# Kernel tuning notes

Measured on AMD Instinct MI355X. Metric: run time of the kernel, lower is better.

The kernel has to match this reference:

```python
import jax, jax.numpy as jnp
import numpy as np

HR, LR, K, RANK = 2048, 1024, 8, 16


def setup_inputs() -> dict:
    key = jax.random.key(0)
    kA, kX, kW, kU, kV, kM = jax.random.split(key, 6)
    A = jax.random.normal(kA, (LR, LR), dtype=jnp.float32)
    A = (A + A.T) / 2  # symmetric so torch UPLO='U' and jax eigh agree
    X = jax.random.normal(kX, (LR, HR), dtype=jnp.float32)
    init_range = (6.0 / (HR + HR)) ** 0.5  # glorot uniform
    weights = jax.random.uniform(kW, (HR, HR), dtype=jnp.float32,
                                 minval=-init_range, maxval=init_range)
    Us = jax.random.normal(kU, (K, HR, RANK), dtype=jnp.float32) * 0.001
    # original inits Vs to zeros; use small noise so corrections are nonzero
    Vs = jax.random.normal(kV, (K, HR, RANK), dtype=jnp.float32) * 0.01
    alphas = jnp.ones((K,), dtype=jnp.float32) / K
    masks = (jax.random.uniform(kM, (K, HR, HR)) < 0.5).astype(jnp.float32)
    return {"A": A, "X": X, "weights": weights, "Us": Us, "Vs": Vs,
            "alphas": alphas, "masks": masks}


def _set_unit_diag(M, eye):
    return M * (1.0 - eye) + eye


def reference(A, X, weights, Us, Vs, alphas, masks):
    lr = A.shape[0]
    hr = weights.shape[0]
    eye_hr = jnp.eye(hr, dtype=A.dtype)
    # --- GSRLayer ---
    _, U_lr = jnp.linalg.eigh(A)                      # (lr, lr)
    s_d = jnp.concatenate([jnp.eye(lr, dtype=A.dtype),
                           jnp.eye(lr, dtype=A.dtype)], axis=0)  # (hr, lr)
    f_d = weights @ s_d @ U_lr.T @ X                  # (hr, hr)
    adj = jnp.abs(f_d)
    adj = _set_unit_diag(adj, eye_hr)
    # --- community-aware low-rank corrections ---
    alpha = jax.nn.softmax(alphas)                    # (k,)
    Zm = adj[None, :, :] * masks                      # (k, hr, hr)
    t = jnp.einsum('kij,kjr->kir', Zm, Us)            # (k, hr, rank)
    corr = jnp.einsum('kir,kjr->kij', t, Vs) * masks  # (k, hr, hr)
    out_adj = adj + jnp.einsum('k,kij->ij', alpha, corr)
    # --- symmetrize with unit diagonal ---
    X_out = out_adj @ out_adj.T
    X_out = (X_out + X_out.T) / 2
    X_out = _set_unit_diag(X_out, eye_hr)
    return out_adj, jnp.abs(X_out)
```

## Files before the change

### kernel.cpp

```cpp
#include <hip/hip_runtime.h>
#include <hip/hip_bf16.h>

typedef unsigned long long u64;

#define MBYTE (1ull << 20)

static const size_t OFF_A64   = 0;
static const size_t OFF_VT    = 8*MBYTE;
static const size_t OFF_TAU   = 12*MBYTE;
static const size_t OFF_D64   = 12*MBYTE +  8192;
static const size_t OFF_E64   = 12*MBYTE + 16384;
static const size_t OFF_XB    = 12*MBYTE + 24576;
static const size_t OFF_Y2B   = 12*MBYTE + 32768;
static const size_t OFF_Y1B   = 12*MBYTE + 40960;
static const size_t OFF_XA    = 12*MBYTE + 49152;
static const size_t OFF_Y1A   = 12*MBYTE + 57344;
static const size_t OFF_Y2A   = 12*MBYTE + 65536;
static const size_t OFF_QA    = 13*MBYTE;
static const size_t OFF_QB    = 17*MBYTE;
static const size_t OFF_SHAT  = 21*MBYTE;
static const size_t OFF_WC    = 25*MBYTE;
static const size_t OFF_M1    = 33*MBYTE;
static const size_t OFF_T8    = 33*MBYTE;
static const size_t OFF_ALPHA = 35*MBYTE + 512*1024;
static const size_t OFF_ADJ   = 41*MBYTE;
static const size_t OFF_OADJ  = 17*MBYTE;
static const size_t OFF_CBUF  = 0;

static const size_t SCD_STRIDE = 9216;
static const size_t SCI_STRIDE = 6144;
static const size_t OFF_SCDB  = OFF_WC;
static const size_t OFF_SCIB  = OFF_WC + 2359296;
static const size_t OFF_KNB   = OFF_WC + 2359296 + 786432;
static const size_t OFF_KNDB  = OFF_WC + 2359296 + 786432 + 2048;


__global__ void kCopyA(const float* __restrict__ A, double* __restrict__ A64) {
  int gid = blockIdx.x*256 + threadIdx.x;
  if (gid < 1024*1024) A64[gid] = (double)A[gid];
}

__device__ __forceinline__ double agLoadD(const double* p) {
  return __hip_atomic_load(p, __ATOMIC_RELAXED, __HIP_MEMORY_SCOPE_AGENT);
}
__device__ __forceinline__ void agStoreD(double* p, double v) {
  __hip_atomic_store(p, v, __ATOMIC_RELAXED, __HIP_MEMORY_SCOPE_AGENT);
}

__global__ __launch_bounds__(1024) void kTriDiag(
    double* __restrict__ A64,
    double* __restrict__ y1A, double* __restrict__ y1B,
    double* __restrict__ y2A, double* __restrict__ y2B,
    double* __restrict__ diagP, unsigned* __restrict__ bar,
    double* __restrict__ tauv, double* __restrict__ e64, double* __restrict__ d64,
    float* __restrict__ Vt) {
  __shared__ double xL[1024], vL[1024], wL[1024], ytL[1024];
  __shared__ double red[4];
  __shared__ double sS[4];
  int tid = threadIdx.x;
  int bid = blockIdx.x;
  bool w0 = (bid == 0);
  int lane = tid & 63, wave = tid >> 6;
  unsigned* barCnt = bar;
  unsigned* barGen = bar + 32;
  const int NBLK = 64;
  int myRow = wave*64 + bid;

  for (int i = 0; i <= 1023; ++i) {
    const double* y1in = (((i-1)&1) != 0) ? y1B : y1A;
    const double* y2in = (((i-1)&1) != 0) ? y2B : y2A;
    double* y1out = ((i&1) != 0) ? y1B : y1A;
    double* y2out = ((i&1) != 0) ? y2B : y2A;

    if (i == 0) {
      if (tid < 256) {
        for (int c = tid; c < 1024; c += 256) { vL[c] = 0.0; wL[c] = 0.0; }
        for (int c = 1 + tid; c < 1024; c += 256) xL[c] = A64[(u64)c*1024];
        if (w0 && tid == 0) d64[0] = A64[0];
      }
      __syncthreads();
    } else {
      int j = i - 1;
      if (tid < 256) {
        double acc = 0.0;
        for (int c = i + 1 + tid; c < 1024; c += 256) { double v = xL[c]; acc += v*v; }
        for (int off = 32; off > 0; off >>= 1) acc += __shfl_xor(acc, off, 64);
        if (lane == 0) red[wave] = acc;
      }
      __syncthreads();
      if (tid == 0) {
        double xn2 = red[0] + red[1] + red[2] + red[3];
        double alpha = xL[i];
        double tv, sc;
        if (xn2 == 0.0) { tv = 0.0; if (w0) e64[j] = alpha; sc = 0.0; }
        else {
          double beta = (alpha >= 0.0) ? -sqrt(alpha*alpha + xn2) : sqrt(alpha*alpha + xn2);
          tv = (beta - alpha)/beta;
          if (w0) e64[j] = beta;
          sc = 1.0/(alpha - beta);
        }
        if (w0) tauv[j] = tv;
        sS[0] = sc; sS[1] = tv;
        vL[i] = 1.0;
        if (w0) Vt[(u64)j*1024 + i] = 1.0f;
      }
      __syncthreads();
      if (tid < 256) {
        double sc = sS[0];
        for (int c = i + 1 + tid; c < 1024; c += 256) {
          double v = xL[c]*sc;
          vL[c] = v;
          if (w0) Vt[(u64)j*1024 + c] = (float)v;
        }
      }
      __syncthreads();
      if (tid < 256) {
        double sc = sS[0], tv = sS[1];
        double acc2 = 0.0;
        for (int r = i + tid; r < 1024; r += 256) {
          double y1v = agLoadD(&y1in[r]);
          double y2v = agLoadD(&y2in[r]);
          ytL[r] = y1v;
          double P = tv*(y1v + sc*y2v);
          wL[r] = P;
          acc2 += P*vL[r];
        }
        for (int off = 32; off > 0; off >>= 1) acc2 += __shfl_xor(acc2, off, 64);
        if (lane == 0) red[wave] = acc2;
      }
      __syncthreads();
      if (tid == 0) sS[2] = 0.5*sS[1]*(red[0] + red[1] + red[2] + red[3]);
      __syncthreads();
      if (tid < 256) {
        double coef = sS[2];
        for (int r = i + tid; r < 1024; r += 256) wL[r] -= coef*vL[r];
      }
      __syncthreads();
      if (tid < 256) {
        double wi = wL[i];
        for (int c = i + 1 + tid; c < 1024; c += 256)
          xL[c] = ytL[c] - vL[c]*wi - wL[c];
        if (tid == 0 && w0) d64[i] = agLoadD(&diagP[i]) - 2.0*wL[i];
      }
      __syncthreads();
    }
    if (i <= 1022) {
      int r = myRow;
      if (r >= i + 1) {
        double vr = vL[r], wr = wL[r];
        double* Arow = A64 + (u64)r*1024;
        double acc = 0.0, y1v = 0.0;
        for (int c = i + 1 + lane; c < 1024; c += 64) {
          double a = Arow[c] - vr*wL[c] - wr*vL[c];
          Arow[c] = a;
          if (c == r) agStoreD(&diagP[r], a);
          if (c == i + 1) y1v = a; else acc += a*xL[c];
        }
        for (int off = 32; off > 0; off >>= 1) acc += __shfl_down(acc, off, 64);
        if (lane == 0) { agStoreD(&y1out[r], y1v); agStoreD(&y2out[r], acc); }
      }
    }
    __syncthreads();
    if (tid == 0) {
      unsigned target = (unsigned)(i + 1);
      unsigned prev = __hip_atomic_fetch_add(barCnt, 1u, __ATOMIC_ACQ_REL, __HIP_MEMORY_SCOPE_AGENT);
      if (prev == (unsigned)(NBLK - 1)) {
        __hip_atomic_store(barCnt, 0u, __ATOMIC_RELAXED, __HIP_MEMORY_SCOPE_AGENT);
        __hip_atomic_store(barGen, target, __ATOMIC_RELEASE, __HIP_MEMORY_SCOPE_AGENT);
      } else {
        while (__hip_atomic_load(barGen, __ATOMIC_ACQUIRE, __HIP_MEMORY_SCOPE_AGENT) < target) {
          __builtin_amdgcn_s_sleep(2);
        }
      }
    }
    __syncthreads();
  }
  if (w0 && tid == 0) {
    for (int c = 16; c < 1024; c += 16) {
      double ae = fabs(e64[c-1]);
      d64[c-1] -= ae;
      d64[c]   -= ae;
    }
  }
}


__device__ void slartg_(double f, double g, double* cs, double* sn, double* r) {
  if (g == 0.0) { *cs = 1.0; *sn = 0.0; *r = f; }
  else if (f == 0.0) { *cs = 0.0; *sn = (g >= 0.0) ? 1.0 : -1.0; *r = fabs(g); }
  else {
    double d = sqrt(f*f + g*g);
    *cs = fabs(f)/d;
    *r = (f >= 0.0) ? d : -d;
    *sn = g / (*r);
  }
}

__device__ void slaev2_(double a, double b, double c, double* rt1, double* rt2,
                        double* cs1, double* sn1) {
  double sm = a + c, df = a - c, adf = fabs(df), tb = b + b, ab = fabs(tb);
  double acmx, acmn;
  if (fabs(a) > fabs(c)) { acmx = a; acmn = c; } else { acmx = c; acmn = a; }
  double rt;
  if (adf > ab) rt = adf*sqrt(1.0 + (ab/adf)*(ab/adf));
  else if (adf < ab) rt = ab*sqrt(1.0 + (adf/ab)*(adf/ab));
  else rt = ab*sqrt(2.0);
  int sgn1;
  if (sm < 0.0) { *rt1 = 0.5*(sm - rt); sgn1 = -1; *rt2 = (acmx / *rt1)*acmn - (b / *rt1)*b; }
  else if (sm > 0.0) { *rt1 = 0.5*(sm + rt); sgn1 = 1; *rt2 = (acmx / *rt1)*acmn - (b / *rt1)*b; }
  else { *rt1 = 0.5*rt; *rt2 = -0.5*rt; sgn1 = 1; }
  int sgn2; double cs;
  if (df >= 0.0) { cs = df + rt; sgn2 = 1; } else { cs = df - rt; sgn2 = -1; }
  double acs = fabs(cs);
  if (acs > ab) { double ct = -tb/cs; *sn1 = 1.0/sqrt(1.0 + ct*ct); *cs1 = ct*(*sn1); }
  else {
    if (ab == 0.0) { *cs1 = 1.0; *sn1 = 0.0; }
    else { double tn = -cs/tb; *cs1 = 1.0/sqrt(1.0 + tn*tn); *sn1 = tn*(*cs1); }
  }
  if (sgn1 == sgn2) { double tn = *cs1; *cs1 = -(*sn1); *sn1 = tn; }
}

__device__ void steqr16_(double* d, double* e, double* z, double* wc, double* ws_) {
  const int n = 16;
  const double eps = 5.9604644775390625e-08;
  const double eps2 = eps*eps;
  const double safmin = 1.1754943508222875e-38;
  int jtot = 0; const int nmaxit = n*30;
  int l1 = 0;
  for (int outer = 0; outer < 200; ++outer) {
    if (l1 > n-1) break;
    if (l1 > 0) e[l1-1] = 0.0;
    int m = l1;
    for (; m <= n-2; ++m) {
      double tst = fabs(e[m]);
      if (tst == 0.0) break;
      if (tst <= (sqrt(fabs(d[m]))*sqrt(fabs(d[m+1])))*eps) { e[m] = 0.0; break; }
    }
    int l = l1, lend = m;
    l1 = m + 1;
    if (lend == l) continue;
    if (fabs(d[lend]) < fabs(d[l])) { int t = l; l = lend; lend = t; }
    if (lend > l) {
      for (int it = 0; it < 800; ++it) {
        int mm = lend;
        if (l != lend) {
          for (mm = l; mm <= lend-1; ++mm) {
            double tst = e[mm]*e[mm];
            if (tst <= eps2*fabs(d[mm])*fabs(d[mm+1]) + safmin) break;
          }
        }
        if (mm < lend) e[mm] = 0.0;
        double p = d[l];
        if (mm == l) { d[l] = p; ++l; if (l <= lend) continue; break; }
        if (mm == l+1) {
          double rt1, rt2, c2, s2;
          slaev2_(d[l], e[l], d[l+1], &rt1, &rt2, &c2, &s2);
          for (int r = 0; r < n; ++r) {
            double t = z[r*16 + l + 1];
            z[r*16 + l + 1] = c2*t - s2*z[r*16 + l];
            z[r*16 + l]     = s2*t + c2*z[r*16 + l];
          }
          d[l] = rt1; d[l+1] = rt2; e[l] = 0.0;
          l += 2; if (l <= lend) continue; break;
        }
        if (jtot == nmaxit) break;
        ++jtot;
        double g = (d[l+1] - p)/(2.0*e[l]);
        double r_ = sqrt(g*g + 1.0);
        g = d[mm] - p + e[l]/(g + ((g >= 0.0) ? r_ : -r_));
        double s = 1.0, c = 1.0;
        p = 0.0;
        for (int i = mm-1; i >= l; --i) {
          double f = s*e[i], b = c*e[i];
          double cs, sn, rr;
          slartg_(g, f, &cs, &sn, &rr);
          c = cs; s = sn;
          if (i != mm-1) e[i+1] = rr;
          g = d[i+1] - p;
          rr = (d[i] - g)*s + 2.0*c*b;
          p = s*rr;
          d[i+1] = g + p;
          g = c*rr - b;
          wc[i] = c; ws_[i] = -s;
        }
        for (int jj = mm-1; jj >= l; --jj) {
          double cs = wc[jj], sn = ws_[jj];
          for (int r = 0; r < n; ++r) {
            double t = z[r*16 + jj + 1];
            z[r*16 + jj + 1] = cs*t - sn*z[r*16 + jj];
            z[r*16 + jj]     = sn*t + cs*z[r*16 + jj];
          }
        }
        d[l] -= p;
        e[l] = g;
      }
    } else {
      for (int it = 0; it < 800; ++it) {
        int mm = lend;
        if (l != lend) {
          for (mm = l; mm >= lend+1; --mm) {
            double tst = e[mm-1]*e[mm-1];
            if (tst <= eps2*fabs(d[mm])*fabs(d[mm-1]) + safmin) break;
          }
        }
        if (mm > lend) e[mm-1] = 0.0;
        double p = d[l];
        if (mm == l) { d[l] = p; --l; if (l >= lend) continue; break; }
        if (mm == l-1) {
          double rt1, rt2, c2, s2;
          slaev2_(d[l-1], e[l-1], d[l], &rt1, &rt2, &c2, &s2);
          for (int r = 0; r < n; ++r) {
            double t = z[r*16 + l];
            z[r*16 + l]     = c2*t - s2*z[r*16 + l - 1];
            z[r*16 + l - 1] = s2*t + c2*z[r*16 + l - 1];
          }
          d[l-1] = rt1; d[l] = rt2; e[l-1] = 0.0;
          l -= 2; if (l >= lend) continue; break;
        }
        if (jtot == nmaxit) break;
        ++jtot;
        double g = (d[l-1] - p)/(2.0*e[l-1]);
        double r_ = sqrt(g*g + 1.0);
        g = d[mm] - p + e[l-1]/(g + ((g >= 0.0) ? r_ : -r_));
        double s = 1.0, c = 1.0;
        p = 0.0;
        for (int i = mm; i <= l-1; ++i) {
          double f = s*e[i], b = c*e[i];
          double cs, sn, rr;
          slartg_(g, f, &cs, &sn, &rr);
          c = cs; s = sn;
          if (i != mm) e[i-1] = rr;
          g = d[i] - p;
          rr = (d[i+1] - g)*s + 2.0*c*b;
          p = s*rr;
          d[i] = g + p;
          g = c*rr - b;
          wc[i] = c; ws_[i] = s;
        }
        for (int jj = mm; jj <= l-1; ++jj) {
          double cs = wc[jj], sn = ws_[jj];
          for (int r = 0; r < n; ++r) {
            double t = z[r*16 + jj + 1];
            z[r*16 + jj + 1] = cs*t - sn*z[r*16 + jj];
            z[r*16 + jj]     = sn*t + cs*z[r*16 + jj];
          }
        }
        d[l] -= p;
        e[l-1] = g;
      }
    }
  }
  for (int ii = 1; ii <= n-1; ++ii) {
    int i = ii - 1, k = i;
    double p = d[i];
    for (int j = ii; j <= n-1; ++j) if (d[j] < p) { k = j; p = d[j]; }
    if (k != i) {
      d[k] = d[i]; d[i] = p;
      for (int r = 0; r < n; ++r) { double t = z[r*16 + i]; z[r*16 + i] = z[r*16 + k]; z[r*16 + k] = t; }
    }
  }
}

__global__ void kLeaf(double* d64, const double* e64, float* Qa) {
  __shared__ double dd[16], ed[16], zd[256], wk1[16], wk2[16];
  int leaf = blockIdx.x, lo = leaf*16, tid = threadIdx.x;
  for (int idx = tid; idx < 256; idx += 64) zd[idx] = ((idx/16) == (idx%16)) ? 1.0 : 0.0;
  if (tid < 16) { dd[tid] = d64[lo + tid]; ed[tid] = (tid < 15) ? e64[lo + tid] : 0.0; }
  __syncthreads();
  if (tid == 0) steqr16_(dd, ed, zd, wk1, wk2);
  __syncthreads();
  for (int idx = tid; idx < 256; idx += 64) {
    int r = idx/16, c = idx%16;
    Qa[(u64)(lo + r)*1024 + lo + c] = (float)zd[idx];
  }
  if (tid < 16) d64[lo + tid] = dd[tid];
}


__global__ __launch_bounds__(1024) void kDeflateB(float* __restrict__ Qa,
      const double* __restrict__ d64, const double* __restrict__ e64,
      double* scdB, int* sciB, int* knB, double* kndB, int bs) {
  __shared__ double zL[1024], dlocL[1024], redD[1024];
  __shared__ double rcL[1024], rsL[1024];
  __shared__ int sIdxL[1024], rpqL[1024];
  __shared__ double sSc[4];
  __shared__ int sKn[4];
  int mg = blockIdx.x;
  int n1 = bs, n = 2*bs, lo = mg*n;
  double* scd = scdB + (u64)mg*SCD_STRIDE;
  int*    sci = sciB + (u64)mg*SCI_STRIDE;
  int* kn = knB + mg*8;
  double* knd = kndB + mg*4;
  int tid = threadIdx.x;
  if (tid == 0) sSc[0] = e64[lo + n1 - 1];
  __syncthreads();
  double rho_in = sSc[0];
  const double invs2 = 0.70710678118654752440;
  if (tid < n) {
    int row = (tid < n1) ? (lo + n1 - 1) : (lo + n1);
    double s = (rho_in < 0.0 && tid >= n1) ? -invs2 : invs2;
    zL[tid] = (double)Qa[(u64)row*1024 + lo + tid] * s;
    dlocL[tid] = d64[lo + tid];
  }
  __syncthreads();
  if (tid < n) {
    int pos; double key = dlocL[tid];
    if (tid < n1) {
      int loB = 0, hiB = n - n1;
      while (loB < hiB) { int mid = (loB+hiB)>>1; if (dlocL[n1+mid] < key) loB = mid+1; else hiB = mid; }
      pos = tid + loB;
    } else {
      int loA = 0, hiA = n1;
      while (loA < hiA) { int mid = (loA+hiA)>>1; if (dlocL[mid] <= key) loA = mid+1; else hiA = mid; }
      pos = (tid - n1) + loA;
    }
    sIdxL[pos] = tid;
  }
  redD[tid] = (tid < n) ? fabs(zL[tid]) : 0.0;
  __syncthreads();
  for (int s = 512; s > 0; s >>= 1) { if (tid < s) redD[tid] = fmax(redD[tid], redD[tid+s]); __syncthreads(); }
  if (tid == 0) sSc[1] = redD[0];
  __syncthreads();
  redD[tid] = (tid < n) ? fabs(dlocL[tid]) : 0.0;
  __syncthreads();
  for (int s = 512; s > 0; s >>= 1) { if (tid < s) redD[tid] = fmax(redD[tid], redD[tid+s]); __syncthreads(); }
  if (tid == 0) {
    double zmax = sSc[1], dmax = redD[0];
    double rho = fabs(2.0*rho_in);
    double tol = 8.0*5.9604644775390625e-8*fmax(dmax, zmax);
    double* dlG = scd + 1024;
    double* wmG = scd + 2048;
    double* dvalG = scd + 7168;
    int* permG = sci;
    int* deflG = sci + 1024;
    int K = 0, nrot = 0, nd = 0; double sw2 = 0.0;
    if (rho*zmax <= tol) {
      for (int pos = 0; pos < n; ++pos) { int c = sIdxL[pos]; deflG[nd] = c; dvalG[nd] = dlocL[c]; nd++; }
    } else {
      int pj = -1, jpos = 0;
      for (; jpos < n; ++jpos) {
        int nj = sIdxL[jpos];
        if (rho*fabs(zL[nj]) <= tol) { deflG[nd] = nj; dvalG[nd] = dlocL[nj]; nd++; }
        else { pj = nj; break; }
      }
      for (++jpos; jpos < n; ++jpos) {
        int nj = sIdxL[jpos];
        if (rho*fabs(zL[nj]) <= tol) { deflG[nd] = nj; dvalG[nd] = dlocL[nj]; nd++; continue; }
        double s_ = zL[pj], c_ = zL[nj];
        double tu = sqrt(c_*c_ + s_*s_);
        double tdif = dlocL[nj] - dlocL[pj];
        c_ /= tu; s_ = -s_/tu;
        if (fabs(tdif*c_*s_) <= tol) {
          zL[nj] = tu; zL[pj] = 0.0;
          rpqL[nrot] = (pj << 16) | nj; rcL[nrot] = c_; rsL[nrot] = s_; nrot++;
          double t1 = dlocL[pj]*c_*c_ + dlocL[nj]*s_*s_;
          dlocL[nj] = dlocL[pj]*s_*s_ + dlocL[nj]*c_*c_;
          dlocL[pj] = t1;
          deflG[nd] = pj; dvalG[nd] = t1; nd++;
          pj = nj;
        } else {
          permG[K] = pj; dlG[K] = dlocL[pj]; wmG[K] = zL[pj]; sw2 += zL[pj]*zL[pj]; K++;
          pj = nj;
        }
      }
      permG[K] = pj; dlG[K] = dlocL[pj]; wmG[K] = zL[pj]; sw2 += zL[pj]*zL[pj]; K++;
    }
    sKn[1] = nrot;
    kn[0] = K; kn[1] = nrot; kn[2] = nd;
    knd[0] = rho; knd[1] = sw2;
  }
  __syncthreads();
  int nrot = sKn[1];
  if (tid < n && nrot > 0) {
    u64 row = (u64)(lo + tid)*1024;
    for (int t = 0; t < nrot; ++t) {
      int pq = rpqL[t];
      int p = lo + (pq >> 16), q = lo + (pq & 0xffff);
      double c = rcL[t], s = rsL[t];
      double x = (double)Qa[row + p], y = (double)Qa[row + q];
      Qa[row + p] = (float)(c*x + s*y);
      Qa[row + q] = (float)(c*y - s*x);
    }
  }
}

__global__ __launch_bounds__(256) void kSecularB(double* scdB, const int* knB, const double* kndB) {
  __shared__ double dlS[1024], wmS[1024];
  int mg = blockIdx.y;
  double* scd = scdB + (u64)mg*SCD_STRIDE;
  const int* kn = knB + mg*8;
  const double* knd = kndB + mg*4;
  int K = kn[0];
  int tid = threadIdx.x;
  for (int j = tid; j < K; j += 256) { dlS[j] = scd[1024 + j]; wmS[j] = scd[2048 + j]; }
  __syncthreads();
  int wave = tid >> 6, lane = tid & 63;
  int i = blockIdx.x*4 + wave;
  if (i >= K) return;
  double rho = knd[0], sw2 = knd[1];
  double di = dlS[i];
  double hi = (i < K-1) ? (dlS[i+1] - di) : (rho*sw2*(1.0 + 1e-12) + 1e-300);
  double lo_ = 0.0;
  for (int it = 0; it < 100; ++it) {
    double mid = 0.5*(lo_ + hi);
    double g = 0.0;
    for (int j = lane; j < K; j += 64) { double w = wmS[j]; g += w*w/((dlS[j] - di) - mid); }
    for (int off = 32; off > 0; off >>= 1) g += __shfl_xor(g, off);
    g = 1.0 + rho*g;
    if (g < 0.0) lo_ = mid; else hi = mid;
  }
  scd[3072 + i] = 0.5*(lo_ + hi);
}

__global__ void kZhatB(double* scdB, const int* knB) {
  int mg = blockIdx.y;
  double* scd = scdB + (u64)mg*SCD_STRIDE;
  int K = (knB + mg*8)[0];
  int j = blockIdx.x*64 + threadIdx.x;
  if (j >= K) return;
  const double* dl = scd + 1024;
  const double* wm = scd + 2048;
  const double* mu = scd + 3072;
  double dj = dl[j];
  double prod = mu[j];
  for (int i2 = 0; i2 < K; ++i2) {
    if (i2 == j) continue;
    double dd = dl[i2] - dj;
    prod *= (dd + mu[i2]) / dd;
  }
  prod = fabs(prod);
  scd[4096 + j] = (wm[j] >= 0.0) ? sqrt(prod) : -sqrt(prod);
}

__global__ __launch_bounds__(1024) void kSortPermB(double* scdB, int* sciB, const int* knB,
                                                   double* d64, int bs) {
  __shared__ double sv[1024];
  __shared__ int si[1024];
  int mg = blockIdx.x;
  int n = 2*bs, lo = mg*n;
  double* scd = scdB + (u64)mg*SCD_STRIDE;
  int* sci = sciB + (u64)mg*SCI_STRIDE;
  int K = (knB + mg*8)[0];
  int tid = threadIdx.x;
  const double* dl = scd + 1024;
  const double* mu = scd + 3072;
  const double* dval = scd + 7168;
  double v;
  if (tid < K) v = dl[tid] + mu[tid];
  else if (tid < n) v = dval[tid - K];
  else v = 1e300;
  sv[tid] = v; si[tid] = tid;
  __syncthreads();
  for (int k = 2; k <= 1024; k <<= 1) {
    for (int j = k >> 1; j > 0; j >>= 1) {
      int ixj = tid ^ j;
      if (ixj > tid) {
        bool up = ((tid & k) == 0);
        double a = sv[tid], b = sv[ixj];
        int ia = si[tid], ib = si[ixj];
        bool agtb = (a > b) || (a == b && ia > ib);
        if (up ? agtb : !agtb) { sv[tid] = b; sv[ixj] = a; si[tid] = ib; si[ixj] = ia; }
      }
      __syncthreads();
    }
  }
  if (tid < n) {
    int s = si[tid];
    if (s < K) sci[4096 + s] = tid; else sci[5120 + s - K] = tid;
    d64[lo + tid] = sv[tid];
  }
}

__global__ void kSvecNormB(float* __restrict__ Shat, const double* scdB, const int* knB, int bs) {
  int mg = blockIdx.y;
  int n = 2*bs, lo = mg*n;
  const double* scd = scdB + (u64)mg*SCD_STRIDE;
  int K = (knB + mg*8)[0];
  int i = blockIdx.x;
  if (i >= K) return;
  const double* dl = scd + 1024;
  const double* mu = scd + 3072;
  const double* zh = scd + 4096;
  __shared__ double red[256];
  int tid = threadIdx.x;
  double di = dl[i], m = mu[i];
  double acc = 0.0;
  for (int j = tid; j < K; j += 256) {
    double v = zh[j]/((dl[j] - di) - m);
    acc += v*v;
  }
  red[tid] = acc; __syncthreads();
  for (int s = 128; s > 0; s >>= 1) { if (tid < s) red[tid] += red[tid+s]; __syncthreads(); }
  double inv = 1.0/sqrt(red[0]);
  for (int j = tid; j < K; j += 256) {
    double v = zh[j]/((dl[j] - di) - m);
    Shat[(u64)j*1024 + lo + i] = (float)(v*inv);
  }
}

__global__ void kGatherB(const float* Qa, float* Qb, const int* sciB, const int* knB, int bs) {
  int mg = blockIdx.y;
  int n = 2*bs, lo = mg*n;
  const int* sci = sciB + (u64)mg*SCI_STRIDE;
  int K = (knB + mg*8)[0];
  int gid = blockIdx.x*256 + threadIdx.x;
  if (gid >= n*n) return;
  int p = gid % n, r = gid / n;
  int src = (p < K) ? sci[p] : sci[1024 + p - K];
  Qb[(u64)(lo + r)*1024 + p] = Qa[(u64)(lo + r)*1024 + lo + src];
}

__global__ void kGemmMergeB(const float* __restrict__ Qb, const float* __restrict__ Shat,
                            float* __restrict__ Qa, const int* sciB, const int* knB, int bs) {
  __shared__ float As[16][17], Bs[16][17];
  int mg = blockIdx.z;
  int n = 2*bs, lo = mg*n;
  const int* sci = sciB + (u64)mg*SCI_STRIDE;
  int K = (knB + mg*8)[0];
  int tx = threadIdx.x, ty = threadIdx.y;
  int r0 = blockIdx.y*16, c0 = blockIdx.x*16;
  const int* rootpos = sci + 4096;
  float acc = 0.f;
  for (int k0 = 0; k0 < K; k0 += 16) {
    As[ty][tx] = (k0 + tx < K) ? Qb[(u64)(lo + r0 + ty)*1024 + k0 + tx] : 0.f;
    Bs[ty][tx] = (k0 + ty < K && c0 + tx < K) ? Shat[(u64)(k0 + ty)*1024 + lo + c0 + tx] : 0.f;
    __syncthreads();
    #pragma unroll
    for (int kk = 0; kk < 16; ++kk) acc += As[ty][kk]*Bs[kk][tx];
    __syncthreads();
  }
  int i = c0 + tx;
  if (i < K) Qa[(u64)(lo + r0 + ty)*1024 + lo + rootpos[i]] = acc;
}

__global__ void kScatterDeflB(const float* Qb, float* Qa, const int* sciB, const int* knB, int bs) {
  int mg = blockIdx.y;
  int n = 2*bs, lo = mg*n;
  const int* sci = sciB + (u64)mg*SCI_STRIDE;
  const int* kn = knB + mg*8;
  int gid = blockIdx.x*256 + threadIdx.x;
  if (gid >= n*n) return;
  int p = gid % n, r = gid / n;
  int K = kn[0], nd = kn[2];
  if (p < K || p - K >= nd) return;
  Qa[(u64)(lo + r)*1024 + lo + sci[5120 + p - K]] = Qb[(u64)(lo + r)*1024 + p];
}

__global__ void kBackx(float* __restrict__ Qa, const float* __restrict__ Vt,
                       const double* __restrict__ tau) {
  __shared__ double red[256];
  __shared__ double stot[16];
  int tid = threadIdx.x;
  int cix = tid & 15, strip = tid >> 4;
  int col = blockIdx.x*16 + cix;
  for (int i = 1022; i >= 0; --i) {
    int m0 = i + 1;
    double s = 0.0;
    for (int r = m0 + strip; r < 1024; r += 16)
      s += (double)Vt[(u64)i*1024 + r] * (double)Qa[(u64)r*1024 + col];
    red[tid] = s;
    __syncthreads();
    if (tid < 16) {
      double tot = 0.0;
      for (int u = 0; u < 16; ++u) tot += red[u*16 + tid];
      stot[tid] = tot * tau[i];
    }
    __syncthreads();
    double f = stot[cix];
    for (int r = m0 + strip; r < 1024; r += 16)
      Qa[(u64)r*1024 + col] -= (float)(f * (double)Vt[(u64)i*1024 + r]);
    __syncthreads();
  }
}


template<int TA, int TB>
__global__ __launch_bounds__(256) void gemm_f32(const float* __restrict__ A,
    const float* __restrict__ B, float* __restrict__ C,
    int M, int N, int Kd, int lda, int ldb, int ldc) {
  __shared__ float As[8][132];
  __shared__ float Bs[8][132];
  int tid = threadIdx.x;
  int bi = blockIdx.y*128, bj = blockIdx.x*128;
  int tx = tid & 15, ty = tid >> 4;
  float acc[8][8];
  #pragma unroll
  for (int x = 0; x < 8; ++x)
    #pragma unroll
    for (int y = 0; y < 8; ++y) acc[x][y] = 0.f;
  for (int k0 = 0; k0 < Kd; k0 += 8) {
    if (TA == 0) {
      int row = tid >> 1, kc = (tid & 1)*4;
      float4 v = *(const float4*)&A[(u64)(bi + row)*lda + k0 + kc];
      As[kc+0][row] = v.x; As[kc+1][row] = v.y; As[kc+2][row] = v.z; As[kc+3][row] = v.w;
    } else {
      int kk = tid >> 5, col = (tid & 31)*4;
      float4 v = *(const float4*)&A[(u64)(k0 + kk)*lda + bi + col];
      *(float4*)&As[kk][col] = v;
    }
    if (TB == 0) {
      int kk = tid >> 5, col = (tid & 31)*4;
      float4 v = *(const float4*)&B[(u64)(k0 + kk)*ldb + bj + col];
      *(float4*)&Bs[kk][col] = v;
    } else {
      int row = tid >> 1, kc = (tid & 1)*4;
      float4 v = *(const float4*)&B[(u64)(bj + row)*ldb + k0 + kc];
      Bs[kc+0][row] = v.x; Bs[kc+1][row] = v.y; Bs[kc+2][row] = v.z; Bs[kc+3][row] = v.w;
    }
    __syncthreads();
    #pragma unroll
    for (int kk = 0; kk < 8; ++kk) {
      float a[8], b[8];
      *(float4*)&a[0] = *(float4*)&As[kk][ty*8];
      *(float4*)&a[4] = *(float4*)&As[kk][ty*8 + 4];
      *(float4*)&b[0] = *(float4*)&Bs[kk][tx*8];
      *(float4*)&b[4] = *(float4*)&Bs[kk][tx*8 + 4];
      #pragma unroll
      for (int x = 0; x < 8; ++x)
        #pragma unroll
        for (int y = 0; y < 8; ++y) acc[x][y] += a[x]*b[y];
    }
    __syncthreads();
  }
  #pragma unroll
  for (int x = 0; x < 8; ++x) {
    float* Crow = &C[(u64)(bi + ty*8 + x)*ldc + bj + tx*8];
    *(float4*)&Crow[0] = make_float4(acc[x][0], acc[x][1], acc[x][2], acc[x][3]);
    *(float4*)&Crow[4] = make_float4(acc[x][4], acc[x][5], acc[x][6], acc[x][7]);
  }
}

__global__ void kWc(const float* W, float* Wc) {
  int gid = blockIdx.x*256 + threadIdx.x;
  if (gid >= 2048*1024) return;
  int i = gid >> 10, k = gid & 1023;
  Wc[gid] = W[(u64)i*2048 + k] + W[(u64)i*2048 + 1024 + k];
}

__global__ void kAbsDiag(float* adj) {
  int gid = blockIdx.x*256 + threadIdx.x;
  if (gid >= 2048*2048) return;
  int i = gid >> 11, j = gid & 2047;
  float v = fabsf(adj[gid]);
  adj[gid] = (i == j) ? 1.0f : v;
}

__global__ void kTk(const float* __restrict__ adj, const float* __restrict__ masks,
                    const float* __restrict__ Us, float* __restrict__ t8) {
  int k = blockIdx.y;
  int i = blockIdx.x*16 + (threadIdx.x >> 4);
  int r = threadIdx.x & 15;
  const float* arow = adj + (u64)i*2048;
  const float* mrow = masks + ((u64)k*2048 + i)*2048;
  const float* uk = Us + (u64)k*2048*16 + r;
  float acc = 0.f;
  for (int j = 0; j < 2048; ++j) acc += arow[j]*mrow[j]*uk[(u64)j*16];
  t8[((u64)k*2048 + i)*16 + r] = acc;
}

__global__ void kAlpha(const float* alphas, float* alpha) {
  if (threadIdx.x == 0 && blockIdx.x == 0) {
    float m = alphas[0];
    for (int k = 1; k < 8; ++k) m = fmaxf(m, alphas[k]);
    float e[8]; float s = 0.f;
    for (int k = 0; k < 8; ++k) { e[k] = expf(alphas[k] - m); s += e[k]; }
    for (int k = 0; k < 8; ++k) alpha[k] = e[k]/s;
  }
}

__global__ void kOutAdj(const float* __restrict__ adj, const float* __restrict__ masks,
                        const float* __restrict__ Vs, const float* __restrict__ t8,
                        const float* __restrict__ alpha, float* __restrict__ oadj,
                        float* __restrict__ out0) {
  __shared__ float tS[8][16][16];
  __shared__ float vS[8][16][16];
  int j0 = blockIdx.x*16, i0 = blockIdx.y*16;
  int tid = threadIdx.x;
  for (int idx = tid; idx < 2048; idx += 256) {
    int k = idx >> 8, rem = idx & 255, row = rem >> 4, r = rem & 15;
    tS[k][row][r] = t8[((u64)k*2048 + i0 + row)*16 + r];
    vS[k][row][r] = Vs[((u64)k*2048 + j0 + row)*16 + r];
  }
  __syncthreads();
  int ii = tid >> 4, jj = tid & 15;
  int i = i0 + ii, j = j0 + jj;
  float corr = 0.f;
  for (int k = 0; k < 8; ++k) {
    float m = masks[((u64)k*2048 + i)*2048 + j];
    float dv = 0.f;
    #pragma unroll
    for (int r = 0; r < 16; ++r) dv += tS[k][ii][r]*vS[k][jj][r];
    corr += alpha[k]*m*dv;
  }
  float val = adj[(u64)i*2048 + j] + corr;
  oadj[(u64)i*2048 + j] = val;
  out0[(u64)i*2048 + j] = val;
}

__global__ void kFinal(const float* __restrict__ C, float* __restrict__ out1) {
  int gid = blockIdx.x*256 + threadIdx.x;
  if (gid >= 2048*2048) return;
  int i = gid >> 11, j = gid & 2047;
  float v;
  if (i == j) v = 1.0f;
  else v = 0.5f*(C[gid] + C[(u64)j*2048 + i]);
  out1[gid] = fabsf(v);
}


extern "C" void kernel_launch(void* const* d_in, const int* in_sizes, int n_in,
                              void* d_out, int out_size, void* d_ws, size_t ws_size,
                              hipStream_t stream) {
  const float* A      = (const float*)d_in[0];
  const float* X      = (const float*)d_in[1];
  const float* W      = (const float*)d_in[2];
  const float* Us     = (const float*)d_in[3];
  const float* Vs     = (const float*)d_in[4];
  const float* alphas = (const float*)d_in[5];
  const float* masks  = (const float*)d_in[6];

  char* ws = (char*)d_ws;
  double* A64  = (double*)(ws + OFF_A64);
  float*  Vt   = (float*) (ws + OFF_VT);
  double* tau  = (double*)(ws + OFF_TAU);
  double* d64  = (double*)(ws + OFF_D64);
  double* e64  = (double*)(ws + OFF_E64);
  double* diagP = (double*)(ws + OFF_XA);
  unsigned* bar = (unsigned*)(ws + OFF_XB);
  double* y1a  = (double*)(ws + OFF_Y1A);
  double* y1b  = (double*)(ws + OFF_Y1B);
  double* y2a  = (double*)(ws + OFF_Y2A);
  double* y2b  = (double*)(ws + OFF_Y2B);
  double* SCDB = (double*)(ws + OFF_SCDB);
  int*    SCIB = (int*)   (ws + OFF_SCIB);
  int*    KNB  = (int*)   (ws + OFF_KNB);
  double* KNDB = (double*)(ws + OFF_KNDB);
  float*  ALPH = (float*) (ws + OFF_ALPHA);
  float*  Qa   = (float*) (ws + OFF_QA);
  float*  Qb   = (float*) (ws + OFF_QB);
  float*  Shat = (float*) (ws + OFF_SHAT);
  float*  Wc   = (float*) (ws + OFF_WC);
  float*  M1   = (float*) (ws + OFF_M1);
  float*  T8   = (float*) (ws + OFF_T8);
  float*  ADJ  = (float*) (ws + OFF_ADJ);
  float*  OADJ = (float*) (ws + OFF_OADJ);
  float*  CB   = (float*) (ws + OFF_CBUF);

  float* out0 = (float*)d_out;
  float* out1 = out0 + (u64)2048*2048;

  hipMemsetAsync(ws + OFF_XB, 0, 256, stream);
  kCopyA<<<4096, 256, 0, stream>>>(A, A64);
  {
    void* kargs[] = { (void*)&A64, (void*)&y1a, (void*)&y1b, (void*)&y2a, (void*)&y2b,
                      (void*)&diagP, (void*)&bar,
                      (void*)&tau, (void*)&e64, (void*)&d64, (void*)&Vt };
    hipLaunchCooperativeKernel((void*)kTriDiag, dim3(64), dim3(1024), kargs, 0, stream);
  }

  hipMemsetAsync(Qa, 0, (size_t)4*MBYTE, stream);
  kLeaf<<<64, 64, 0, stream>>>(d64, e64, Qa);

  for (int lvl = 0; lvl < 6; ++lvl) {
    int bs = 16 << lvl;
    int n = 2*bs;
    int cnt = 1024/n;
    kDeflateB<<<cnt, 1024, 0, stream>>>(Qa, d64, e64, SCDB, SCIB, KNB, KNDB, bs);
    kSecularB<<<dim3((n + 3)/4, cnt), 256, 0, stream>>>(SCDB, KNB, KNDB);
    kZhatB<<<dim3((n + 63)/64, cnt), 64, 0, stream>>>(SCDB, KNB);
    kSortPermB<<<cnt, 1024, 0, stream>>>(SCDB, SCIB, KNB, d64, bs);
    kSvecNormB<<<dim3(n, cnt), 256, 0, stream>>>(Shat, SCDB, KNB, bs);
    kGatherB<<<dim3((n*n + 255)/256, cnt), 256, 0, stream>>>(Qa, Qb, SCIB, KNB, bs);
    kGemmMergeB<<<dim3(n/16, n/16, cnt), dim3(16, 16), 0, stream>>>(Qb, Shat, Qa, SCIB, KNB, bs);
    kScatterDeflB<<<dim3((n*n + 255)/256, cnt), 256, 0, stream>>>(Qb, Qa, SCIB, KNB, bs);
  }

  kBackx<<<64, 256, 0, stream>>>(Qa, Vt, tau);

  kWc<<<8192, 256, 0, stream>>>(W, Wc);
  gemm_f32<1,0><<<dim3(16, 8), 256, 0, stream>>>(Qa, X, M1, 1024, 2048, 1024, 1024, 2048, 2048);
  gemm_f32<0,0><<<dim3(16, 16), 256, 0, stream>>>(Wc, M1, ADJ, 2048, 2048, 1024, 1024, 2048, 2048);
  kAbsDiag<<<16384, 256, 0, stream>>>(ADJ);
  kTk<<<dim3(128, 8), 256, 0, stream>>>(ADJ, masks, Us, T8);
  kAlpha<<<1, 64, 0, stream>>>(alphas, ALPH);
  kOutAdj<<<dim3(128, 128), 256, 0, stream>>>(ADJ, masks, Vs, T8, ALPH, OADJ, out0);
  gemm_f32<0,1><<<dim3(16, 16), 256, 0, stream>>>(OADJ, OADJ, CB, 2048, 2048, 2048, 2048, 2048, 2048);
  kFinal<<<16384, 256, 0, stream>>>(CB, out1);
}
```

Measured before the change: 20.90 ms.

## Restructure tridiagonal reduction grid, use flag barrier, and pair Householder back-transforms

The cooperative tridiagonalisation kernel moves from 64 blocks of 1024 threads (only 256 of them active in the per-step vector phase) to 256 blocks of 256 threads. It replaces the counter/generation grid barrier with per-block flags that a single wave polls, prefetches the y vectors before the norm reduction, and merges several of the per-step shared-memory phases so fewer __syncthreads are needed. The row update loop is unrolled four-wide. The back-transformation kernel applies two Householder reflectors per pass, which halves the number of sequential sweeps over Qa at the cost of an extra dot product and more register use.

```diff
diff --git a/kernel.cpp b/kernel.cpp
--- a/kernel.cpp
+++ b/kernel.cpp
@@ -47,24 +47,23 @@
   __hip_atomic_store(p, v, __ATOMIC_RELAXED, __HIP_MEMORY_SCOPE_AGENT);
 }
 
-__global__ __launch_bounds__(1024) void kTriDiag(
+#define TD_NBLK 256
+
+__global__ __launch_bounds__(256) void kTriDiag(
     double* __restrict__ A64,
     double* __restrict__ y1A, double* __restrict__ y1B,
     double* __restrict__ y2A, double* __restrict__ y2B,
-    double* __restrict__ diagP, unsigned* __restrict__ bar,
+    double* __restrict__ diagP, unsigned* __restrict__ flags,
     double* __restrict__ tauv, double* __restrict__ e64, double* __restrict__ d64,
     float* __restrict__ Vt) {
-  __shared__ double xL[1024], vL[1024], wL[1024], ytL[1024];
+  __shared__ double xL[1024], vL[1024], wL[1024], y1L[1024], y2L[1024];
   __shared__ double red[4];
   __shared__ double sS[4];
   int tid = threadIdx.x;
   int bid = blockIdx.x;
   bool w0 = (bid == 0);
   int lane = tid & 63, wave = tid >> 6;
-  unsigned* barCnt = bar;
-  unsigned* barGen = bar + 32;
-  const int NBLK = 64;
-  int myRow = wave*64 + bid;
+  int myRow = wave*TD_NBLK + bid;
 
   for (int i = 0; i <= 1023; ++i) {
     const double* y1in = (((i-1)&1) != 0) ? y1B : y1A;
@@ -73,20 +72,26 @@
     double* y2out = ((i&1) != 0) ? y2B : y2A;
 
     if (i == 0) {
-      if (tid < 256) {
-        for (int c = tid; c < 1024; c += 256) { vL[c] = 0.0; wL[c] = 0.0; }
-        for (int c = 1 + tid; c < 1024; c += 256) xL[c] = A64[(u64)c*1024];
-        if (w0 && tid == 0) d64[0] = A64[0];
-      }
+      for (int c = tid; c < 1024; c += 256) { vL[c] = 0.0; wL[c] = 0.0; }
+      for (int c = 1 + tid; c < 1024; c += 256) xL[c] = A64[(u64)c*1024];
+      if (w0 && tid == 0) d64[0] = A64[0];
       __syncthreads();
     } else {
       int j = i - 1;
-      if (tid < 256) {
-        double acc = 0.0;
-        for (int c = i + 1 + tid; c < 1024; c += 256) { double v = xL[c]; acc += v*v; }
-        for (int off = 32; off > 0; off >>= 1) acc += __shfl_xor(acc, off, 64);
-        if (lane == 0) red[wave] = acc;
-      }
+      double a1[4], a2[4];
+      #pragma unroll
+      for (int k = 0; k < 4; ++k) {
+        a1[k] = agLoadD(&y1in[tid + 256*k]);
+        a2[k] = agLoadD(&y2in[tid + 256*k]);
+      }
+      double dg = 0.0;
+      if (w0 && tid == 0) dg = agLoadD(&diagP[i]);
+      double acc = 0.0;
+      for (int c = i + 1 + tid; c < 1024; c += 256) { double v = xL[c]; acc += v*v; }
+      for (int off = 32; off > 0; off >>= 1) acc += __shfl_xor(acc, off, 64);
+      if (lane == 0) red[wave] = acc;
+      #pragma unroll
+      for (int k = 0; k < 4; ++k) { y1L[tid + 256*k] = a1[k]; y2L[tid + 256*k] = a2[k]; }
       __syncthreads();
       if (tid == 0) {
         double xn2 = red[0] + red[1] + red[2] + red[3];
@@ -105,42 +110,39 @@
         if (w0) Vt[(u64)j*1024 + i] = 1.0f;
       }
       __syncthreads();
-      if (tid < 256) {
-        double sc = sS[0];
-        for (int c = i + 1 + tid; c < 1024; c += 256) {
-          double v = xL[c]*sc;
-          vL[c] = v;
-          if (w0) Vt[(u64)j*1024 + c] = (float)v;
-        }
-      }
-      __syncthreads();
-      if (tid < 256) {
+      {
         double sc = sS[0], tv = sS[1];
         double acc2 = 0.0;
         for (int r = i + tid; r < 1024; r += 256) {
-          double y1v = agLoadD(&y1in[r]);
-          double y2v = agLoadD(&y2in[r]);
-          ytL[r] = y1v;
-          double P = tv*(y1v + sc*y2v);
+          double v;
+          if (r == i) v = 1.0;
+          else {
+            v = xL[r]*sc;
+            vL[r] = v;
+            if (w0) Vt[(u64)j*1024 + r] = (float)v;
+          }
+          double P = tv*(y1L[r] + sc*y2L[r]);
           wL[r] = P;
-          acc2 += P*vL[r];
+          acc2 += P*v;
         }
         for (int off = 32; off > 0; off >>= 1) acc2 += __shfl_xor(acc2, off, 64);
         if (lane == 0) red[wave] = acc2;
       }
       __syncthreads();
-      if (tid == 0) sS[2] = 0.5*sS[1]*(red[0] + red[1] + red[2] + red[3]);
+      if (tid == 0) {
+        double coef = 0.5*sS[1]*(red[0] + red[1] + red[2] + red[3]);
+        double wi = wL[i] - coef;
+        sS[2] = coef; sS[3] = wi;
+        if (w0) d64[i] = dg - 2.0*wi;
+      }
       __syncthreads();
-      if (tid < 256) {
-        double coef = sS[2];
-        for (int r = i + tid; r < 1024; r += 256) wL[r] -= coef*vL[r];
-      }
-      __syncthreads();
-      if (tid < 256) {
-        double wi = wL[i];
-        for (int c = i + 1 + tid; c < 1024; c += 256)
-          xL[c] = ytL[c] - vL[c]*wi - wL[c];
-        if (tid == 0 && w0) d64[i] = agLoadD(&diagP[i]) - 2.0*wL[i];
+      {
+        double coef = sS[2], wi = sS[3];
+        for (int r = i + tid; r < 1024; r += 256) {
+          double wcr = wL[r] - coef*vL[r];
+          wL[r] = wcr;
+          if (r > i) xL[r] = y1L[r] - vL[r]*wi - wcr;
+        }
       }
       __syncthreads();
     }
@@ -150,7 +152,27 @@
         double vr = vL[r], wr = wL[r];
         double* Arow = A64 + (u64)r*1024;
         double acc = 0.0, y1v = 0.0;
-        for (int c = i + 1 + lane; c < 1024; c += 64) {
+        int c = i + 1 + lane;
+        for (; c + 192 < 1024; c += 256) {
+          double A0 = Arow[c], A1 = Arow[c+64], A2 = Arow[c+128], A3 = Arow[c+192];
+          double w0_ = wL[c], w1_ = wL[c+64], w2_ = wL[c+128], w3_ = wL[c+192];
+          double v0_ = vL[c], v1_ = vL[c+64], v2_ = vL[c+128], v3_ = vL[c+192];
+          double x0_ = xL[c], x1_ = xL[c+64], x2_ = xL[c+128], x3_ = xL[c+192];
+          double b0 = A0 - vr*w0_ - wr*v0_;
+          double b1 = A1 - vr*w1_ - wr*v1_;
+          double b2 = A2 - vr*w2_ - wr*v2_;
+          double b3 = A3 - vr*w3_ - wr*v3_;
+          Arow[c] = b0; Arow[c+64] = b1; Arow[c+128] = b2; Arow[c+192] = b3;
+          if (c == r)     agStoreD(&diagP[r], b0);
+          if (c+64 == r)  agStoreD(&diagP[r], b1);
+          if (c+128 == r) agStoreD(&diagP[r], b2);
+          if (c+192 == r) agStoreD(&diagP[r], b3);
+          if (c == i + 1) y1v = b0; else acc += b0*x0_;
+          acc += b1*x1_;
+          acc += b2*x2_;
+          acc += b3*x3_;
+        }
+        for (; c < 1024; c += 64) {
           double a = Arow[c] - vr*wL[c] - wr*vL[c];
           Arow[c] = a;
           if (c == r) agStoreD(&diagP[r], a);
@@ -159,21 +181,25 @@
         for (int off = 32; off > 0; off >>= 1) acc += __shfl_down(acc, off, 64);
         if (lane == 0) { agStoreD(&y1out[r], y1v); agStoreD(&y2out[r], acc); }
       }
-    }
-    __syncthreads();
-    if (tid == 0) {
-      unsigned target = (unsigned)(i + 1);
-      unsigned prev = __hip_atomic_fetch_add(barCnt, 1u, __ATOMIC_ACQ_REL, __HIP_MEMORY_SCOPE_AGENT);
-      if (prev == (unsigned)(NBLK - 1)) {
-        __hip_atomic_store(barCnt, 0u, __ATOMIC_RELAXED, __HIP_MEMORY_SCOPE_AGENT);
-        __hip_atomic_store(barGen, target, __ATOMIC_RELEASE, __HIP_MEMORY_SCOPE_AGENT);
-      } else {
-        while (__hip_atomic_load(barGen, __ATOMIC_ACQUIRE, __HIP_MEMORY_SCOPE_AGENT) < target) {
+      __syncthreads();
+      unsigned tgt = (unsigned)(i + 1);
+      if (tid == 0)
+        __hip_atomic_store(&flags[bid], tgt, __ATOMIC_RELEASE, __HIP_MEMORY_SCOPE_AGENT);
+      if (tid < 64) {
+        for (;;) {
+          unsigned m0 = __hip_atomic_load(&flags[tid      ], __ATOMIC_ACQUIRE, __HIP_MEMORY_SCOPE_AGENT);
+          unsigned m1 = __hip_atomic_load(&flags[tid +  64], __ATOMIC_ACQUIRE, __HIP_MEMORY_SCOPE_AGENT);
+          unsigned m2 = __hip_atomic_load(&flags[tid + 128], __ATOMIC_ACQUIRE, __HIP_MEMORY_SCOPE_AGENT);
+          unsigned m3 = __hip_atomic_load(&flags[tid + 192], __ATOMIC_ACQUIRE, __HIP_MEMORY_SCOPE_AGENT);
+          unsigned ma = (m0 < m1) ? m0 : m1;
+          unsigned mb = (m2 < m3) ? m2 : m3;
+          unsigned mn = (ma < mb) ? ma : mb;
+          if (__all(mn >= tgt)) break;
           __builtin_amdgcn_s_sleep(2);
         }
       }
-    }
-    __syncthreads();
+      __syncthreads();
+    }
   }
   if (w0 && tid == 0) {
     for (int c = 16; c < 1024; c += 16) {
@@ -648,28 +674,63 @@
 
 __global__ void kBackx(float* __restrict__ Qa, const float* __restrict__ Vt,
                        const double* __restrict__ tau) {
-  __shared__ double red[256];
-  __shared__ double stot[16];
+  __shared__ double redA[256], redB[256], redS[16];
+  __shared__ double fA[16], fB[16];
   int tid = threadIdx.x;
   int cix = tid & 15, strip = tid >> 4;
   int col = blockIdx.x*16 + cix;
-  for (int i = 1022; i >= 0; --i) {
-    int m0 = i + 1;
-    double s = 0.0;
-    for (int r = m0 + strip; r < 1024; r += 16)
-      s += (double)Vt[(u64)i*1024 + r] * (double)Qa[(u64)r*1024 + col];
-    red[tid] = s;
+  for (int a = 1022; a >= 2; a -= 2) {
+    int b = a - 1;
+    double ta = tau[a], tb = tau[b];
+    const float* va_row = Vt + (u64)a*1024;
+    const float* vb_row = Vt + (u64)b*1024;
+    double pda = 0.0, pdb = 0.0, ps = 0.0;
+    for (int r = a + strip; r < 1024; r += 16) {
+      double zb = (double)Qa[(u64)r*1024 + col];
+      double va = (r > a) ? (double)va_row[r] : 0.0;
+      double vb = (double)vb_row[r];
+      pda += va*zb; pdb += vb*zb;
+      if (cix == 0) ps += va*vb;
+    }
+    redA[tid] = pda; redB[tid] = pdb;
+    if (cix == 0) redS[strip] = ps;
     __syncthreads();
     if (tid < 16) {
-      double tot = 0.0;
-      for (int u = 0; u < 16; ++u) tot += red[u*16 + tid];
-      stot[tid] = tot * tau[i];
+      double da = 0.0, db = 0.0, s = 0.0;
+      for (int u = 0; u < 16; ++u) {
+        da += redA[u*16 + tid];
+        db += redB[u*16 + tid];
+        s  += redS[u];
+      }
+      fA[tid] = ta*da;
+      fB[tid] = tb*(db - ta*s*da);
     }
     __syncthreads();
-    double f = stot[cix];
-    for (int r = m0 + strip; r < 1024; r += 16)
-      Qa[(u64)r*1024 + col] -= (float)(f * (double)Vt[(u64)i*1024 + r]);
+    double fa = fA[cix], fb = fB[cix];
+    for (int r = a + strip; r < 1024; r += 16) {
+      double va = (r > a) ? (double)va_row[r] : 0.0;
+      double vb = (double)vb_row[r];
+      Qa[(u64)r*1024 + col] -= (float)(fa*va + fb*vb);
+    }
     __syncthreads();
+  }
+  {
+    double t0 = tau[0];
+    const float* v_row = Vt;
+    double pd = 0.0;
+    for (int r = 1 + strip; r < 1024; r += 16)
+      pd += (double)v_row[r] * (double)Qa[(u64)r*1024 + col];
+    redA[tid] = pd;
+    __syncthreads();
+    if (tid < 16) {
+      double d = 0.0;
+      for (int u = 0; u < 16; ++u) d += redA[u*16 + tid];
+      fA[tid] = t0*d;
+    }
+    __syncthreads();
+    double f = fA[cix];
+    for (int r = 1 + strip; r < 1024; r += 16)
+      Qa[(u64)r*1024 + col] -= (float)(f * (double)v_row[r]);
   }
 }
 
@@ -826,7 +887,7 @@
   double* d64  = (double*)(ws + OFF_D64);
   double* e64  = (double*)(ws + OFF_E64);
   double* diagP = (double*)(ws + OFF_XA);
-  unsigned* bar = (unsigned*)(ws + OFF_XB);
+  unsigned* flags = (unsigned*)(ws + OFF_XB);
   double* y1a  = (double*)(ws + OFF_Y1A);
   double* y1b  = (double*)(ws + OFF_Y1B);
   double* y2a  = (double*)(ws + OFF_Y2A);
@@ -849,13 +910,13 @@
   float* out0 = (float*)d_out;
   float* out1 = out0 + (u64)2048*2048;
 
-  hipMemsetAsync(ws + OFF_XB, 0, 256, stream);
+  hipMemsetAsync(ws + OFF_XB, 0, 1024, stream);
   kCopyA<<<4096, 256, 0, stream>>>(A, A64);
   {
     void* kargs[] = { (void*)&A64, (void*)&y1a, (void*)&y1b, (void*)&y2a, (void*)&y2b,
-                      (void*)&diagP, (void*)&bar,
+                      (void*)&diagP, (void*)&flags,
                       (void*)&tau, (void*)&e64, (void*)&d64, (void*)&Vt };
-    hipLaunchCooperativeKernel((void*)kTriDiag, dim3(64), dim3(1024), kargs, 0, stream);
+    hipLaunchCooperativeKernel((void*)kTriDiag, dim3(TD_NBLK), dim3(256), kargs, 0, stream);
   }
 
   hipMemsetAsync(Qa, 0, (size_t)4*MBYTE, stream);
```

Result: slower. 38.32 ms (+83.4%).
